# Optimization experiments

Measured on AMD Instinct MI355X. Metric: run time of the kernel, lower is better.

Reference implementation:

```python
import jax, jax.numpy as jnp
import numpy as np

D_MODEL = 1024
NHEAD = 16
D_HEAD = D_MODEL // NHEAD


def setup_inputs() -> dict:
    key = jax.random.key(0)
    ks = jax.random.split(key, 5)
    s_in = 1.0 / np.sqrt(D_MODEL)
    x = jax.random.normal(ks[0], (2, 2048, D_MODEL), dtype=jnp.float32)
    Wqkv = jax.random.uniform(ks[1], (D_MODEL, 3 * D_MODEL), jnp.float32, -s_in, s_in)
    bqkv = jax.random.uniform(ks[2], (3 * D_MODEL,), jnp.float32, -s_in, s_in)
    Wproj = jax.random.uniform(ks[3], (D_MODEL, D_MODEL), jnp.float32, -s_in, s_in)
    bproj = jax.random.uniform(ks[4], (D_MODEL,), jnp.float32, -s_in, s_in)
    return {"x": x, "Wqkv": Wqkv, "bqkv": bqkv, "Wproj": Wproj, "bproj": bproj}


def reference(x, Wqkv, bqkv, Wproj, bproj):
    B, N, D = x.shape
    qkv = x @ Wqkv + bqkv                       # [B, N, 3D]
    q, k, v = jnp.split(qkv, 3, axis=-1)
    # [B, N, D] -> [B, H, N, d]
    def to_heads(t):
        return t.reshape(B, N, NHEAD, D_HEAD).transpose(0, 2, 1, 3)
    q, k, v = to_heads(q), to_heads(k), to_heads(v)
    scale = 1.0 / np.sqrt(D_HEAD).astype(np.float32)
    attn = jnp.einsum('bhqd,bhkd->bhqk', q, k) * scale
    attn = jax.nn.softmax(attn, axis=-1)
    y = jnp.einsum('bhqk,bhkd->bhqd', attn, v)  # [B, H, N, d]
    y = y.transpose(0, 2, 1, 3).reshape(B, N, D)
    return y @ Wproj + bproj
```

## Files before the change

kernel.cpp:

```cpp
#include <hip/hip_runtime.h>
#include <hip/hip_bf16.h>
#include <stdint.h>

typedef __hip_bfloat16 bf16;
typedef __attribute__((ext_vector_type(8))) short short8;
typedef __attribute__((ext_vector_type(4))) float f32x4;

#define QSCALE 0.18033688011f

__device__ __forceinline__ float fast_exp2(float x) {
#if __has_builtin(__builtin_amdgcn_exp2f)
  return __builtin_amdgcn_exp2f(x);
#else
  return exp2f(x);
#endif
}

__device__ __forceinline__ uint32_t pack2_bf16(float a, float b) {
#if __has_builtin(__builtin_amdgcn_cvt_pk_bf16_f32)
  typedef __attribute__((ext_vector_type(2))) __bf16 bf16x2;
  bf16x2 v = __builtin_amdgcn_cvt_pk_bf16_f32(a, b);
  return __builtin_bit_cast(uint32_t, v);
#else
  uint32_t ua = __builtin_bit_cast(uint32_t, a);
  uint32_t ub = __builtin_bit_cast(uint32_t, b);
  ua += 0x7FFF + ((ua >> 16) & 1);
  ub += 0x7FFF + ((ub >> 16) & 1);
  return (ua >> 16) | (ub & 0xFFFF0000u);
#endif
}

__device__ __forceinline__ void gload_lds16(const bf16* g, bf16* l) {
#if __has_builtin(__builtin_amdgcn_global_load_lds)
  __builtin_amdgcn_global_load_lds(
      (const __attribute__((address_space(1))) void*)(uintptr_t)g,
      (__attribute__((address_space(3))) void*)(uint32_t)(uintptr_t)l,
      16, 0, 0);
#else
  int lane = threadIdx.x & 63;
  *(short8*)(l + lane * 8) = *(const short8*)(g + lane * 8);
#endif
}

__device__ __forceinline__ void lds_barrier() {
  asm volatile("s_waitcnt lgkmcnt(0)\n\ts_barrier" ::: "memory");
}

__device__ __forceinline__ void transpose_tile(const float* __restrict__ in,
                                               bf16* __restrict__ out,
                                               int R, int C, int bx, int by,
                                               bf16 (*t)[72]) {
  const int r0 = by * 64, c0 = bx * 64;
  const int rr = threadIdx.x >> 3, cc = (threadIdx.x & 7) * 8;
#pragma unroll
  for (int rep = 0; rep < 2; ++rep) {
    int y = rr + rep * 32;
    const float* p = in + (size_t)(r0 + y) * C + c0 + cc;
    f32x4 v0 = *(const f32x4*)p;
    f32x4 v1 = *(const f32x4*)(p + 4);
#pragma unroll
    for (int j = 0; j < 4; ++j) {
      t[cc + j][y] = __float2bfloat16(v0[j]);
      t[cc + 4 + j][y] = __float2bfloat16(v1[j]);
    }
  }
  __syncthreads();
#pragma unroll
  for (int rep = 0; rep < 2; ++rep) {
    int y = rr + rep * 32;
    short8 v = *(const short8*)&t[y][cc];
    *(short8*)(out + (size_t)(c0 + y) * R + r0 + cc) = v;
  }
}

__global__ __launch_bounds__(256)
void prep_k(const float* __restrict__ x, bf16* __restrict__ xb,
            const float* __restrict__ Wqkv, bf16* __restrict__ WtQkv,
            const float* __restrict__ Wproj, bf16* __restrict__ WtP) {
  __shared__ __align__(16) bf16 t[64][72];
  const int bid = blockIdx.x;
  if (bid < 2048) {
    int i = (bid * 256 + threadIdx.x) * 8;
    f32x4 v0 = *(const f32x4*)(x + i);
    f32x4 v1 = *(const f32x4*)(x + i + 4);
    short8 r;
    bf16* rb = (bf16*)&r;
#pragma unroll
    for (int j = 0; j < 4; ++j) {
      rb[j] = __float2bfloat16(v0[j]);
      rb[4 + j] = __float2bfloat16(v1[j]);
    }
    *(short8*)(xb + i) = r;
  } else if (bid < 2048 + 768) {
    int b = bid - 2048;
    transpose_tile(Wqkv, WtQkv, 1024, 3072, b % 48, b / 48, t);
  } else {
    int b = bid - 2816;
    transpose_tile(Wproj, WtP, 1024, 1024, b % 16, b / 16, t);
  }
}

template <int MODE, int TM>
__global__ __launch_bounds__(256, 2)
void gemm_bt(const bf16* __restrict__ A, const bf16* __restrict__ Bt,
             const float* __restrict__ bias, float* __restrict__ outp,
             bf16* __restrict__ Qd, bf16* __restrict__ Kd, bf16* __restrict__ Vt,
             int M, int Nn, int K) {
  constexpr int MI = TM / 32;
  __shared__ __align__(16) bf16 smem[(TM == 128) ? 9216 : 6144];
  bf16* As = smem;
  bf16* Bs = smem + TM * 32;

  const int tid = threadIdx.x;
  const int wave = tid >> 6, lane = tid & 63;
  const int quad = lane >> 4, l16 = lane & 15;
  const int mw = (wave >> 1) * (TM / 2), nw = (wave & 1) * 64;
  const int m_blk = blockIdx.y * TM, n_blk = blockIdx.x * 128;

  f32x4 acc[MI][4];
#pragma unroll
  for (int i = 0; i < MI; ++i)
#pragma unroll
    for (int j = 0; j < 4; ++j) acc[i][j] = (f32x4){0.f, 0.f, 0.f, 0.f};

  const int rowA = lane >> 2, colA = (lane & 3) * 8;
  const int chunkB = wave * 2;
  const bf16* gB = Bt + (size_t)(n_blk + chunkB * 16 + rowA) * K + colA;
  bf16* lB0 = &Bs[chunkB * 16 * 32];
  bf16* lB1 = &Bs[(chunkB + 1) * 16 * 32];

  const int chunkA = (TM == 128) ? wave * 2 : wave;
  const bf16* gA = A + (size_t)(m_blk + chunkA * 16 + rowA) * K + colA;
  bf16* lA0 = &As[chunkA * 16 * 32];
  bf16* lA1 = &As[(chunkA + 1) * 16 * 32];

  for (int kt = 0; kt < K; kt += 32) {
    gload_lds16(gA, lA0);
    if (TM == 128) gload_lds16(gA + 16 * K, lA1);
    gload_lds16(gB, lB0);
    gload_lds16(gB + 16 * K, lB1);
    gA += 32; gB += 32;
    __syncthreads();
    short8 af[MI], bfv[4];
#pragma unroll
    for (int i = 0; i < MI; ++i)
      af[i] = *(const short8*)&As[(mw + i * 16 + l16) * 32 + quad * 8];
#pragma unroll
    for (int j = 0; j < 4; ++j)
      bfv[j] = *(const short8*)&Bs[(nw + j * 16 + l16) * 32 + quad * 8];
#pragma unroll
    for (int i = 0; i < MI; ++i)
#pragma unroll
      for (int j = 0; j < 4; ++j)
        acc[i][j] = __builtin_amdgcn_mfma_f32_16x16x32_bf16(af[i], bfv[j],
                                                            acc[i][j], 0, 0, 0);
    __syncthreads();
  }

  if (MODE == 0) {
    float bval[4];
#pragma unroll
    for (int j = 0; j < 4; ++j) bval[j] = bias[n_blk + nw + j * 16 + l16];

    const int part = n_blk >> 10;
    const int b = m_blk >> 11;
    const int tloc = m_blk & 2047;
    const int h0 = (n_blk & 1023) >> 6;

#pragma unroll
    for (int p = 0; p < 2; ++p) {
      __syncthreads();
      if ((nw >> 6) == p) {
        if (part == 2) {
#pragma unroll
          for (int i = 0; i < MI; ++i)
#pragma unroll
            for (int j = 0; j < 4; ++j) {
              const int dh = j * 16 + l16;
              const int t0 = mw + i * 16 + quad * 4;
              uint2 pk;
              pk.x = pack2_bf16(acc[i][j][0] + bval[j], acc[i][j][1] + bval[j]);
              pk.y = pack2_bf16(acc[i][j][2] + bval[j], acc[i][j][3] + bval[j]);
              *(uint2*)&smem[dh * 136 + t0] = pk;
            }
        } else {
          const float sc = (part == 0) ? QSCALE : 1.0f;
#pragma unroll
          for (int i = 0; i < MI; ++i)
#pragma unroll
            for (int j = 0; j < 4; ++j) {
              const int d = j * 16 + l16;
              const int t0 = mw + i * 16 + quad * 4;
#pragma unroll
              for (int r = 0; r < 4; ++r)
                smem[(t0 + r) * 72 + d] =
                    __float2bfloat16((acc[i][j][r] + bval[j]) * sc);
            }
        }
      }
      __syncthreads();
      const size_t bh = (size_t)(b * 16 + h0 + p);
      if (part == 2) {
#pragma unroll
        for (int it = 0; it < 4; ++it) {
          const int dl = (tid >> 4) + it * 16;
          const int t8 = (tid & 15) * 8;
          short8 v = *(const short8*)&smem[dl * 136 + t8];
          *(short8*)&Vt[(bh * 64 + dl) * 2048 + tloc + t8] = v;
        }
      } else {
        bf16* dst = (part == 0) ? Qd : Kd;
#pragma unroll
        for (int it = 0; it < 4; ++it) {
          const int row = (tid >> 3) + it * 32;
          const int col8 = (tid & 7) * 8;
          short8 v = *(const short8*)&smem[row * 72 + col8];
          *(short8*)&dst[(bh * 2048 + tloc + row) * 64 + col8] = v;
        }
      }
    }
  } else {
#pragma unroll
    for (int j = 0; j < 4; ++j) {
      const int ncol = n_blk + nw + j * 16 + l16;
      const float bval = bias[ncol];
#pragma unroll
      for (int i = 0; i < MI; ++i) {
        const int mrow0 = m_blk + mw + i * 16 + quad * 4;
#pragma unroll
        for (int r = 0; r < 4; ++r)
          outp[(size_t)(mrow0 + r) * Nn + ncol] = acc[i][j][r] + bval;
      }
    }
  }
}

__global__ __launch_bounds__(256, 2)
void attn_kernel(const bf16* __restrict__ Qg, const bf16* __restrict__ Kg,
                 const bf16* __restrict__ Vt, bf16* __restrict__ yg) {
  __shared__ __align__(16) char pool[71680];
  bf16* KsB = (bf16*)pool;
  bf16* VtsB = (bf16*)(pool + 36864);

  const int tid = threadIdx.x;
  const int wave = tid >> 6, lane = tid & 63;
  const int quad = lane >> 4, l16 = lane & 15;

  const int bx = blockIdx.x;
  const int qt = bx & 31;
  const int bh = bx >> 5;

  const bf16* Qb = Qg + ((size_t)bh * 2048 + qt * 64) * 64;
  const bf16* Kb = Kg + (size_t)bh * 2048 * 64;
  const bf16* Vtb = Vt + (size_t)bh * 64 * 2048;

  short8 qf[4][2];
#pragma unroll
  for (int qblk = 0; qblk < 4; ++qblk)
#pragma unroll
    for (int ks = 0; ks < 2; ++ks)
      qf[qblk][ks] = *(const short8*)(
          Qb + (size_t)(qblk * 16 + l16) * 64 + ks * 32 + quad * 8);

  const int kr = tid >> 3, kc = (tid & 7) * 8;
  const int vdd = tid & 63, vo = tid >> 6;
  const bf16* Kp = Kb + (size_t)kr * 64 + kc;
  const bf16* Vp = Vtb + (size_t)vdd * 2048 + vo * 8;
  int vws[4];
#pragma unroll
  for (int j = 0; j < 4; ++j)
    vws[j] = vdd * 136 + (((vo + 4 * j) + (vdd >> 3)) & 15) * 8;

#pragma unroll
  for (int j = 0; j < 4; ++j) {
    short8 a = *(const short8*)(Kp + (size_t)(32 * j) * 64);
    *(short8*)(KsB + (kr + 32 * j) * 72 + kc) = a;
  }
#pragma unroll
  for (int j = 0; j < 4; ++j) {
    short8 c = *(const short8*)(Vp + j * 32);
    *(short8*)(VtsB + vws[j]) = c;
  }
  short8 gk[4], gv[4];
#pragma unroll
  for (int j = 0; j < 4; ++j)
    gk[j] = *(const short8*)(Kp + (size_t)(128 + 32 * j) * 64);
#pragma unroll
  for (int j = 0; j < 4; ++j)
    gv[j] = *(const short8*)(Vp + 128 + j * 32);
  __syncthreads();

  f32x4 yacc[4][4];
#pragma unroll
  for (int qblk = 0; qblk < 4; ++qblk)
#pragma unroll
    for (int dblk = 0; dblk < 4; ++dblk)
      yacc[qblk][dblk] = (f32x4){0.f, 0.f, 0.f, 0.f};
  f32x4 sum_acc[4];
#pragma unroll
  for (int qblk = 0; qblk < 4; ++qblk)
    sum_acc[qblk] = (f32x4){0.f, 0.f, 0.f, 0.f};

  uint4 ones_u;
  ones_u.x = ones_u.y = ones_u.z = ones_u.w = 0x3F803F80u;
  const short8 ones8 = __builtin_bit_cast(short8, ones_u);

  const int kfo = (wave * 32 + l16) * 72 + quad * 8;
  int vbo[4][2];
#pragma unroll
  for (int dblk = 0; dblk < 4; ++dblk) {
    const int d = dblk * 16 + l16;
#pragma unroll
    for (int kvblk = 0; kvblk < 2; ++kvblk) {
      const int c = wave * 4 + kvblk * 2 + (quad >> 1);
      vbo[dblk][kvblk] = d * 136 + ((c + (d >> 3)) & 15) * 8 + (quad & 1) * 4;
    }
  }

  for (int kt = 0; kt < 2048; kt += 128) {
    const int cur = (kt >> 7) & 1;
    bf16* KsC = KsB + cur * 9216;
    bf16* VtsC = VtsB + cur * 8704;

    if (kt + 128 < 2048) {
      bf16* KsN = KsB + (cur ^ 1) * 9216;
      bf16* VtsN = VtsB + (cur ^ 1) * 8704;
#pragma unroll
      for (int j = 0; j < 4; ++j)
        *(short8*)(KsN + (kr + 32 * j) * 72 + kc) = gk[j];
#pragma unroll
      for (int j = 0; j < 4; ++j)
        *(short8*)(VtsN + vws[j]) = gv[j];
      if (kt + 256 < 2048) {
#pragma unroll
        for (int j = 0; j < 4; ++j)
          gk[j] = *(const short8*)(Kp + (size_t)(kt + 256 + 32 * j) * 64);
#pragma unroll
        for (int j = 0; j < 4; ++j)
          gv[j] = *(const short8*)(Vp + kt + 256 + j * 32);
      }
    }

    short8 kf[2][2];
#pragma unroll
    for (int kvblk = 0; kvblk < 2; ++kvblk)
#pragma unroll
      for (int ks = 0; ks < 2; ++ks)
        kf[kvblk][ks] =
            *(const short8*)(KsC + kfo + kvblk * 16 * 72 + ks * 32);
    uint2 vlo[4], vhi[4];
#pragma unroll
    for (int dblk = 0; dblk < 4; ++dblk) {
      vlo[dblk] = *(const uint2*)(VtsC + vbo[dblk][0]);
      vhi[dblk] = *(const uint2*)(VtsC + vbo[dblk][1]);
    }

    short8 pa8[4];
#pragma unroll
    for (int qblk = 0; qblk < 4; ++qblk) {
      f32x4 s0 = (f32x4){0.f, 0.f, 0.f, 0.f};
      f32x4 s1 = (f32x4){0.f, 0.f, 0.f, 0.f};
      s0 = __builtin_amdgcn_mfma_f32_16x16x32_bf16(kf[0][0], qf[qblk][0], s0, 0, 0, 0);
      s0 = __builtin_amdgcn_mfma_f32_16x16x32_bf16(kf[0][1], qf[qblk][1], s0, 0, 0, 0);
      s1 = __builtin_amdgcn_mfma_f32_16x16x32_bf16(kf[1][0], qf[qblk][0], s1, 0, 0, 0);
      s1 = __builtin_amdgcn_mfma_f32_16x16x32_bf16(kf[1][1], qf[qblk][1], s1, 0, 0, 0);
      float p0 = fast_exp2(s0[0]), p1 = fast_exp2(s0[1]);
      float p2 = fast_exp2(s0[2]), p3 = fast_exp2(s0[3]);
      float p4 = fast_exp2(s1[0]), p5 = fast_exp2(s1[1]);
      float p6 = fast_exp2(s1[2]), p7 = fast_exp2(s1[3]);
      uint4 u;
      u.x = pack2_bf16(p0, p1);
      u.y = pack2_bf16(p2, p3);
      u.z = pack2_bf16(p4, p5);
      u.w = pack2_bf16(p6, p7);
      pa8[qblk] = __builtin_bit_cast(short8, u);
      sum_acc[qblk] = __builtin_amdgcn_mfma_f32_16x16x32_bf16(
          pa8[qblk], ones8, sum_acc[qblk], 0, 0, 0);
    }

#pragma unroll
    for (int dblk = 0; dblk < 4; ++dblk) {
      uint4 u;
      u.x = vlo[dblk].x; u.y = vlo[dblk].y;
      u.z = vhi[dblk].x; u.w = vhi[dblk].y;
      short8 vb8 = __builtin_bit_cast(short8, u);
#pragma unroll
      for (int qblk = 0; qblk < 4; ++qblk)
        yacc[qblk][dblk] = __builtin_amdgcn_mfma_f32_16x16x32_bf16(
            pa8[qblk], vb8, yacc[qblk][dblk], 0, 0, 0);
    }

    lds_barrier();
  }

  __syncthreads();
  float* red = (float*)pool;
  if (wave != 0) {
    float* buf = red + (wave - 1) * 4160;
#pragma unroll
    for (int qblk = 0; qblk < 4; ++qblk) {
#pragma unroll
      for (int dblk = 0; dblk < 4; ++dblk)
        *(f32x4*)&buf[((qblk * 4 + dblk) * 64 + lane) * 4] = yacc[qblk][dblk];
      if (l16 == 0)
        *(f32x4*)&buf[4096 + qblk * 16 + quad * 4] = sum_acc[qblk];
    }
  }
  __syncthreads();
  if (wave == 0) {
#pragma unroll
    for (int w = 0; w < 3; ++w) {
      float* buf = red + w * 4160;
#pragma unroll
      for (int qblk = 0; qblk < 4; ++qblk) {
        f32x4 sp = *(const f32x4*)&buf[4096 + qblk * 16 + quad * 4];
#pragma unroll
        for (int r = 0; r < 4; ++r) sum_acc[qblk][r] += sp[r];
#pragma unroll
        for (int dblk = 0; dblk < 4; ++dblk) {
          f32x4 o = *(const f32x4*)&buf[((qblk * 4 + dblk) * 64 + lane) * 4];
#pragma unroll
          for (int r = 0; r < 4; ++r) yacc[qblk][dblk][r] += o[r];
        }
      }
    }
    const int b = bh >> 4, h = bh & 15;
    const size_t rowbase = (size_t)b * 2048 + qt * 64;
#pragma unroll
    for (int qblk = 0; qblk < 4; ++qblk) {
#pragma unroll
      for (int r = 0; r < 4; ++r) {
        const float inv = 1.f / sum_acc[qblk][r];
        const int rr = qblk * 16 + quad * 4 + r;
#pragma unroll
        for (int dblk = 0; dblk < 4; ++dblk)
          yg[(rowbase + rr) * 1024 + h * 64 + dblk * 16 + l16] =
              __float2bfloat16(yacc[qblk][dblk][r] * inv);
      }
    }
  }
}

extern "C" void kernel_launch(void* const* d_in, const int* in_sizes, int n_in,
                              void* d_out, int out_size, void* d_ws, size_t ws_size,
                              hipStream_t stream) {
  const float* x = (const float*)d_in[0];
  const float* Wqkv = (const float*)d_in[1];
  const float* bqkv = (const float*)d_in[2];
  const float* Wproj = (const float*)d_in[3];
  const float* bproj = (const float*)d_in[4];
  float* out = (float*)d_out;

  if (ws_size < (size_t)40 * 1024 * 1024) return;

  char* ws = (char*)d_ws;
  bf16* xb    = (bf16*)(ws + 0);
  bf16* yd    = (bf16*)(ws + 0);
  bf16* WtQkv = (bf16*)(ws + 8388608);
  bf16* WtP   = (bf16*)(ws + 14680064);
  bf16* Qd    = (bf16*)(ws + 16777216);
  bf16* Kd    = (bf16*)(ws + 25165824);
  bf16* Vten  = (bf16*)(ws + 33554432);

  prep_k<<<3072, 256, 0, stream>>>(x, xb, Wqkv, WtQkv, Wproj, WtP);
  gemm_bt<0, 128><<<dim3(24, 32), 256, 0, stream>>>(
      xb, WtQkv, bqkv, nullptr, Qd, Kd, Vten, 4096, 3072, 1024);
  attn_kernel<<<dim3(1024), 256, 0, stream>>>(Qd, Kd, Vten, yd);
  gemm_bt<1, 64><<<dim3(8, 64), 256, 0, stream>>>(
      yd, WtP, bproj, out, nullptr, nullptr, nullptr, 4096, 1024, 1024);
}
```

Measured before the change: 202.2 us.

## Halve attention query tile and single-buffer K/V LDS to raise occupancy

The attention kernel now processes 32 query rows per block instead of 64, doubling the grid to 2048 blocks. K/V shared memory goes from double-buffered to single-buffered, with an extra barrier after fragments are read and before the next tile is written. This cuts LDS and register use so launch bounds allow three blocks per CU, aiming to hide latency through occupancy. In exchange, each K/V tile loaded from global memory now serves half as many query rows, and every iteration carries an additional barrier.

```diff
diff --git a/kernel.cpp b/kernel.cpp
--- a/kernel.cpp
+++ b/kernel.cpp
@@ -235,28 +235,28 @@
   }
 }
 
-__global__ __launch_bounds__(256, 2)
+__global__ __launch_bounds__(256, 3)
 void attn_kernel(const bf16* __restrict__ Qg, const bf16* __restrict__ Kg,
                  const bf16* __restrict__ Vt, bf16* __restrict__ yg) {
-  __shared__ __align__(16) char pool[71680];
-  bf16* KsB = (bf16*)pool;
-  bf16* VtsB = (bf16*)(pool + 36864);
+  __shared__ __align__(16) char pool[35840];
+  bf16* Ks = (bf16*)pool;
+  bf16* Vts = (bf16*)(pool + 18432);
 
   const int tid = threadIdx.x;
   const int wave = tid >> 6, lane = tid & 63;
   const int quad = lane >> 4, l16 = lane & 15;
 
   const int bx = blockIdx.x;
-  const int qt = bx & 31;
-  const int bh = bx >> 5;
-
-  const bf16* Qb = Qg + ((size_t)bh * 2048 + qt * 64) * 64;
+  const int qt = bx & 63;
+  const int bh = bx >> 6;
+
+  const bf16* Qb = Qg + ((size_t)bh * 2048 + qt * 32) * 64;
   const bf16* Kb = Kg + (size_t)bh * 2048 * 64;
   const bf16* Vtb = Vt + (size_t)bh * 64 * 2048;
 
-  short8 qf[4][2];
-#pragma unroll
-  for (int qblk = 0; qblk < 4; ++qblk)
+  short8 qf[2][2];
+#pragma unroll
+  for (int qblk = 0; qblk < 2; ++qblk)
 #pragma unroll
     for (int ks = 0; ks < 2; ++ks)
       qf[qblk][ks] = *(const short8*)(
@@ -274,12 +274,12 @@
 #pragma unroll
   for (int j = 0; j < 4; ++j) {
     short8 a = *(const short8*)(Kp + (size_t)(32 * j) * 64);
-    *(short8*)(KsB + (kr + 32 * j) * 72 + kc) = a;
+    *(short8*)(Ks + (kr + 32 * j) * 72 + kc) = a;
   }
 #pragma unroll
   for (int j = 0; j < 4; ++j) {
     short8 c = *(const short8*)(Vp + j * 32);
-    *(short8*)(VtsB + vws[j]) = c;
+    *(short8*)(Vts + vws[j]) = c;
   }
   short8 gk[4], gv[4];
 #pragma unroll
@@ -290,16 +290,15 @@
     gv[j] = *(const short8*)(Vp + 128 + j * 32);
   __syncthreads();
 
-  f32x4 yacc[4][4];
-#pragma unroll
-  for (int qblk = 0; qblk < 4; ++qblk)
+  f32x4 yacc[2][4];
+#pragma unroll
+  for (int qblk = 0; qblk < 2; ++qblk)
 #pragma unroll
     for (int dblk = 0; dblk < 4; ++dblk)
       yacc[qblk][dblk] = (f32x4){0.f, 0.f, 0.f, 0.f};
-  f32x4 sum_acc[4];
-#pragma unroll
-  for (int qblk = 0; qblk < 4; ++qblk)
-    sum_acc[qblk] = (f32x4){0.f, 0.f, 0.f, 0.f};
+  f32x4 sum_acc[2];
+  sum_acc[0] = (f32x4){0.f, 0.f, 0.f, 0.f};
+  sum_acc[1] = (f32x4){0.f, 0.f, 0.f, 0.f};
 
   uint4 ones_u;
   ones_u.x = ones_u.y = ones_u.z = ones_u.w = 0x3F803F80u;
@@ -318,19 +317,32 @@
   }
 
   for (int kt = 0; kt < 2048; kt += 128) {
-    const int cur = (kt >> 7) & 1;
-    bf16* KsC = KsB + cur * 9216;
-    bf16* VtsC = VtsB + cur * 8704;
+    short8 kf[2][2];
+#pragma unroll
+    for (int kvblk = 0; kvblk < 2; ++kvblk)
+#pragma unroll
+      for (int ks = 0; ks < 2; ++ks)
+        kf[kvblk][ks] =
+            *(const short8*)(Ks + kfo + kvblk * 16 * 72 + ks * 32);
+    short8 vb8[4];
+#pragma unroll
+    for (int dblk = 0; dblk < 4; ++dblk) {
+      uint2 lo = *(const uint2*)(Vts + vbo[dblk][0]);
+      uint2 hi = *(const uint2*)(Vts + vbo[dblk][1]);
+      uint4 u;
+      u.x = lo.x; u.y = lo.y; u.z = hi.x; u.w = hi.y;
+      vb8[dblk] = __builtin_bit_cast(short8, u);
+    }
+
+    lds_barrier();
 
     if (kt + 128 < 2048) {
-      bf16* KsN = KsB + (cur ^ 1) * 9216;
-      bf16* VtsN = VtsB + (cur ^ 1) * 8704;
 #pragma unroll
       for (int j = 0; j < 4; ++j)
-        *(short8*)(KsN + (kr + 32 * j) * 72 + kc) = gk[j];
+        *(short8*)(Ks + (kr + 32 * j) * 72 + kc) = gk[j];
 #pragma unroll
       for (int j = 0; j < 4; ++j)
-        *(short8*)(VtsN + vws[j]) = gv[j];
+        *(short8*)(Vts + vws[j]) = gv[j];
       if (kt + 256 < 2048) {
 #pragma unroll
         for (int j = 0; j < 4; ++j)
@@ -341,23 +353,9 @@
       }
     }
 
-    short8 kf[2][2];
-#pragma unroll
-    for (int kvblk = 0; kvblk < 2; ++kvblk)
-#pragma unroll
-      for (int ks = 0; ks < 2; ++ks)
-        kf[kvblk][ks] =
-            *(const short8*)(KsC + kfo + kvblk * 16 * 72 + ks * 32);
-    uint2 vlo[4], vhi[4];
-#pragma unroll
-    for (int dblk = 0; dblk < 4; ++dblk) {
-      vlo[dblk] = *(const uint2*)(VtsC + vbo[dblk][0]);
-      vhi[dblk] = *(const uint2*)(VtsC + vbo[dblk][1]);
-    }
-
-    short8 pa8[4];
-#pragma unroll
-    for (int qblk = 0; qblk < 4; ++qblk) {
+    short8 pa8[2];
+#pragma unroll
+    for (int qblk = 0; qblk < 2; ++qblk) {
       f32x4 s0 = (f32x4){0.f, 0.f, 0.f, 0.f};
       f32x4 s1 = (f32x4){0.f, 0.f, 0.f, 0.f};
       s0 = __builtin_amdgcn_mfma_f32_16x16x32_bf16(kf[0][0], qf[qblk][0], s0, 0, 0, 0);
@@ -380,14 +378,10 @@
 
 #pragma unroll
     for (int dblk = 0; dblk < 4; ++dblk) {
-      uint4 u;
-      u.x = vlo[dblk].x; u.y = vlo[dblk].y;
-      u.z = vhi[dblk].x; u.w = vhi[dblk].y;
-      short8 vb8 = __builtin_bit_cast(short8, u);
-#pragma unroll
-      for (int qblk = 0; qblk < 4; ++qblk)
-        yacc[qblk][dblk] = __builtin_amdgcn_mfma_f32_16x16x32_bf16(
-            pa8[qblk], vb8, yacc[qblk][dblk], 0, 0, 0);
+      yacc[0][dblk] = __builtin_amdgcn_mfma_f32_16x16x32_bf16(
+          pa8[0], vb8[dblk], yacc[0][dblk], 0, 0, 0);
+      yacc[1][dblk] = __builtin_amdgcn_mfma_f32_16x16x32_bf16(
+          pa8[1], vb8[dblk], yacc[1][dblk], 0, 0, 0);
     }
 
     lds_barrier();
@@ -396,24 +390,24 @@
   __syncthreads();
   float* red = (float*)pool;
   if (wave != 0) {
-    float* buf = red + (wave - 1) * 4160;
-#pragma unroll
-    for (int qblk = 0; qblk < 4; ++qblk) {
+    float* buf = red + (wave - 1) * 2080;
+#pragma unroll
+    for (int qblk = 0; qblk < 2; ++qblk) {
 #pragma unroll
       for (int dblk = 0; dblk < 4; ++dblk)
         *(f32x4*)&buf[((qblk * 4 + dblk) * 64 + lane) * 4] = yacc[qblk][dblk];
       if (l16 == 0)
-        *(f32x4*)&buf[4096 + qblk * 16 + quad * 4] = sum_acc[qblk];
+        *(f32x4*)&buf[2048 + qblk * 16 + quad * 4] = sum_acc[qblk];
     }
   }
   __syncthreads();
   if (wave == 0) {
 #pragma unroll
     for (int w = 0; w < 3; ++w) {
-      float* buf = red + w * 4160;
-#pragma unroll
-      for (int qblk = 0; qblk < 4; ++qblk) {
-        f32x4 sp = *(const f32x4*)&buf[4096 + qblk * 16 + quad * 4];
+      float* buf = red + w * 2080;
+#pragma unroll
+      for (int qblk = 0; qblk < 2; ++qblk) {
+        f32x4 sp = *(const f32x4*)&buf[2048 + qblk * 16 + quad * 4];
 #pragma unroll
         for (int r = 0; r < 4; ++r) sum_acc[qblk][r] += sp[r];
 #pragma unroll
@@ -425,9 +419,9 @@
       }
     }
     const int b = bh >> 4, h = bh & 15;
-    const size_t rowbase = (size_t)b * 2048 + qt * 64;
-#pragma unroll
-    for (int qblk = 0; qblk < 4; ++qblk) {
+    const size_t rowbase = (size_t)b * 2048 + qt * 32;
+#pragma unroll
+    for (int qblk = 0; qblk < 2; ++qblk) {
 #pragma unroll
       for (int r = 0; r < 4; ++r) {
         const float inv = 1.f / sum_acc[qblk][r];
@@ -465,7 +459,7 @@
   prep_k<<<3072, 256, 0, stream>>>(x, xb, Wqkv, WtQkv, Wproj, WtP);
   gemm_bt<0, 128><<<dim3(24, 32), 256, 0, stream>>>(
       xb, WtQkv, bqkv, nullptr, Qd, Kd, Vten, 4096, 3072, 1024);
-  attn_kernel<<<dim3(1024), 256, 0, stream>>>(Qd, Kd, Vten, yd);
+  attn_kernel<<<dim3(2048), 256, 0, stream>>>(Qd, Kd, Vten, yd);
   gemm_bt<1, 64><<<dim3(8, 64), 256, 0, stream>>>(
       yd, WtP, bproj, out, nullptr, nullptr, nullptr, 4096, 1024, 1024);
 }
```

New measurement: 225.7 us. +11.6%, slower.
